# Performance work log

Hardware: AMD Instinct MI355X
Metric: run time of the kernel (lower is better)

## Reference

```python
import jax, jax.numpy as jnp
import numpy as np

B, N0, FEAT, NHID, GDIM = 32, 2048, 1036, 128, 32
DEG = 16
E = B * N0 * DEG
K1, K2, K3 = 410, 82, 17  # ceil(0.2*{2048,410,82}) per SAGPooling stage


def _segsum(v, idx, n):
    return jax.ops.segment_sum(v, idx, num_segments=n)


def sage_conv(x, src, dst, em, Wl, bl, Wr, n):
    # PyG SAGEConv: lin_l(mean_{j->i} x_j) + lin_r(x_i); lin applied before the
    # (linear) mean -> identical math, messages are NHID-dim not FEAT-dim.
    h = x @ Wl
    s = _segsum(h[src] * em[:, None], dst, n)
    cnt = _segsum(em, dst, n)
    return s / jnp.maximum(cnt, 1.0)[:, None] + bl + x @ Wr


def gcn_score(x, src, dst, em, W, b, n):
    # 1-channel GCNConv with self-loops and symmetric normalization.
    h = x @ W  # [n, 1]
    deg = 1.0 + _segsum(em, dst, n)  # +1 for self loop
    dis = jax.lax.rsqrt(deg)
    norm = dis[src] * dis[dst] * em
    agg = _segsum(h[src] * norm[:, None], dst, n) + h / deg[:, None]
    return (agg + b)[:, 0]


def sag_pool(x, src, dst, em, W, b, n_per, k):
    # Equal-size graphs -> static top-k per graph; dropped edges masked, not removed.
    nb = x.shape[0] // n_per
    score = gcn_score(x, src, dst, em, W, b, x.shape[0])
    _, idx = jax.lax.top_k(score.reshape(nb, n_per), k)
    perm = (idx + (jnp.arange(nb) * n_per)[:, None]).reshape(-1)
    xn = x[perm] * jnp.tanh(score[perm])[:, None]
    inv = jnp.full((x.shape[0],), -1, jnp.int32).at[perm].set(
        jnp.arange(nb * k, dtype=jnp.int32))
    ns, nd = inv[src], inv[dst]
    emn = em * ((ns >= 0) & (nd >= 0)).astype(em.dtype)
    return xn, jnp.maximum(ns, 0), jnp.maximum(nd, 0), emn


def readout(x, k):
    r = x.reshape(B, k, NHID)
    return jnp.concatenate([r.max(axis=1), r.mean(axis=1)], axis=1)  # [B, 2*NHID]


def graphnet(x, src, dst, W1l, b1l, W1r, Wp1, bp1, W2l, b2l, W2r, Wp2, bp2,
             W3l, b3l, W3r, Wp3, bp3, lin1_w, lin1_b, lin2_w, lin2_b, lin3_w, lin3_b):
    # NormalizeFeaturesV2: first 12 cols / column max
    mx = jnp.max(x[:, :12], axis=0)
    x = jnp.concatenate([x[:, :12] / mx, x[:, 12:]], axis=1)
    em = jnp.ones((E,), x.dtype)

    x = jax.nn.relu(sage_conv(x, src, dst, em, W1l, b1l, W1r, B * N0))
    x, s1, d1, e1 = sag_pool(x, src, dst, em, Wp1, bp1, N0, K1)
    x1 = readout(x, K1)

    x = jax.nn.relu(sage_conv(x, s1, d1, e1, W2l, b2l, W2r, B * K1))
    x, s2, d2, e2 = sag_pool(x, s1, d1, e1, Wp2, bp2, K1, K2)
    x2 = readout(x, K2)

    x = jax.nn.relu(sage_conv(x, s2, d2, e2, W3l, b3l, W3r, B * K2))
    x, s3, d3, e3 = sag_pool(x, s2, d2, e2, Wp3, bp3, K2, K3)
    x3 = readout(x, K3)

    h = x1 + x2 + x3
    h = jax.nn.relu(h @ lin1_w + lin1_b)  # dropout is identity at eval
    features = jax.nn.relu(h @ lin2_w + lin2_b)
    out = features @ lin3_w + lin3_b  # act=None
    return features, out


def setup_inputs():
    key = jax.random.key(0)
    ks = jax.random.split(key, 16)
    x = jax.random.normal(ks[0], (B * N0, FEAT), jnp.float32)
    e = jax.random.randint(ks[1], (2, B, N0 * DEG), 0, N0)
    ei = (e + (jnp.arange(B) * N0)[None, :, None]).reshape(2, -1).astype(jnp.int32)

    def lin(k, fi, fo):
        return (jax.random.normal(k, (fi, fo), jnp.float32) / np.sqrt(fi)).astype(jnp.float32)

    z = lambda *s: jnp.zeros(s, jnp.float32)
    return dict(
        x=x, src=ei[0], dst=ei[1],
        W1l=lin(ks[2], FEAT, NHID), b1l=z(NHID), W1r=lin(ks[3], FEAT, NHID),
        Wp1=lin(ks[4], NHID, 1), bp1=z(1),
        W2l=lin(ks[5], NHID, NHID), b2l=z(NHID), W2r=lin(ks[6], NHID, NHID),
        Wp2=lin(ks[7], NHID, 1), bp2=z(1),
        W3l=lin(ks[8], NHID, NHID), b3l=z(NHID), W3r=lin(ks[9], NHID, NHID),
        Wp3=lin(ks[10], NHID, 1), bp3=z(1),
        lin1_w=lin(ks[11], 2 * NHID, NHID), lin1_b=z(NHID),
        lin2_w=lin(ks[12], NHID, GDIM), lin2_b=z(GDIM),
        lin3_w=lin(ks[13], GDIM, 1), lin3_b=z(1),
    )


def reference(x, src, dst, W1l, b1l, W1r, Wp1, bp1, W2l, b2l, W2r, Wp2, bp2,
              W3l, b3l, W3r, Wp3, bp3, lin1_w, lin1_b, lin2_w, lin2_b, lin3_w, lin3_b):
    return graphnet(x, src, dst, W1l, b1l, W1r, Wp1, bp1, W2l, b2l, W2r, Wp2, bp2,
                    W3l, b3l, W3r, Wp3, bp3, lin1_w, lin1_b, lin2_w, lin2_b,
                    lin3_w, lin3_b)
```

## Files before the change

kernel.cpp:

```cpp
#include <hip/hip_runtime.h>

typedef unsigned int u32;
typedef unsigned short u16;

#define NB 32
#define N0V 2048
#define FEATV 1036
#define EDGESV (NB*N0V*16)
#define KK1 410
#define KK2 82
#define KK3 17
#define NN1 (NB*N0V)
#define NN2 (NB*KK1)
#define NN3 (NB*KK2)
#define NN4 (NB*KK3)
#define KSTEP1 33
#define KSTEP2 4
#define ESTR 32768

typedef __bf16 bf16x8 __attribute__((ext_vector_type(8)));
typedef float f32x4 __attribute__((ext_vector_type(4)));

__device__ inline u16 f2bf(float f){
  u32 u = __float_as_uint(f);
  u32 r = (u + 0x7FFFu + ((u >> 16) & 1u)) >> 16;
  return (u16)r;
}
__device__ inline float bf2f(u16 h){ return __uint_as_float(((u32)h) << 16); }
__device__ inline float dec_ord(u32 u){
  u32 bits = (u & 0x80000000u) ? (u ^ 0x80000000u) : ~u;
  return __uint_as_float(bits);
}
__device__ inline u16 bfbits(__bf16 b){ union{__bf16 f; u16 u;} c; c.f=b; return c.u; }
__device__ inline void cvt4c(float4 v, ushort4& h, ushort4& l){
  __bf16 h0=(__bf16)v.x, h1=(__bf16)v.y, h2=(__bf16)v.z, h3=(__bf16)v.w;
  float r0=v.x-(float)h0, r1=v.y-(float)h1, r2=v.z-(float)h2, r3=v.w-(float)h3;
  h.x=bfbits(h0); h.y=bfbits(h1); h.z=bfbits(h2); h.w=bfbits(h3);
  l.x=bfbits((__bf16)r0); l.y=bfbits((__bf16)r1);
  l.z=bfbits((__bf16)r2); l.w=bfbits((__bf16)r3);
}
__device__ inline void gload_lds16(const void* g, void* l){
  __builtin_amdgcn_global_load_lds(
      (const __attribute__((address_space(1))) unsigned int*)g,
      (__attribute__((address_space(3))) unsigned int*)l, 16, 0, 0);
}

__global__ void init_kernel(u32* mx){
  if (threadIdx.x < 12) mx[threadIdx.x] = 0;
}

__global__ void colmax_kernel(const float* __restrict__ x, u32* mx){
  __shared__ float sm[256];
  int t = threadIdx.x;
  int r = blockIdx.x*256 + t;
  const float4* p = (const float4*)(x + (size_t)r*FEATV);
  float4 v0 = p[0], v1 = p[1], v2 = p[2];
  float m[12] = {v0.x,v0.y,v0.z,v0.w, v1.x,v1.y,v1.z,v1.w, v2.x,v2.y,v2.z,v2.w};
  for (int j=0;j<12;j++){
    sm[t] = m[j]; __syncthreads();
    for (int off=128; off>0; off>>=1){ if (t<off) sm[t]=fmaxf(sm[t],sm[t+off]); __syncthreads(); }
    if (t==0){
      u32 b = __float_as_uint(sm[0]);
      u32 u = (b & 0x80000000u) ? ~b : (b | 0x80000000u);
      atomicMax(&mx[j], u);
    }
    __syncthreads();
  }
}

__global__ void wprep_all(const float* __restrict__ W1l, const float* __restrict__ W1r,
                          const float* __restrict__ W2l, const float* __restrict__ W2r,
                          const float* __restrict__ W3l, const float* __restrict__ W3r,
                          const u32* __restrict__ mxo,
                          u16* __restrict__ B1h, u16* __restrict__ B1l,
                          u16* __restrict__ B2h, u16* __restrict__ B2l,
                          u16* __restrict__ B3h, u16* __restrict__ B3l){
  int idx = blockIdx.x*256 + threadIdx.x;
  const float *Wl, *Wr; u16 *oh, *ol; int K, o, scale12;
  if (idx < KSTEP1*8192){ Wl=W1l; Wr=W1r; oh=B1h; ol=B1l; K=FEATV; o=idx; scale12=1; }
  else if (idx < (KSTEP1+KSTEP2)*8192){ Wl=W2l; Wr=W2r; oh=B2h; ol=B2l; K=128; o=idx-KSTEP1*8192; scale12=0; }
  else if (idx < (KSTEP1+2*KSTEP2)*8192){ Wl=W3l; Wr=W3r; oh=B3h; ol=B3l; K=128; o=idx-(KSTEP1+KSTEP2)*8192; scale12=0; }
  else return;
  int kt = o >> 13, r13 = o & 8191;
  int khg = r13 >> 11, n = (r13 >> 3) & 255, kk8 = r13 & 7;
  int k = (kt << 5) + khg*8 + kk8;
  float v = 0.f;
  if (k < K) v = (n < 128) ? Wl[(size_t)k*128 + n] : Wr[(size_t)k*128 + (n-128)];
  if (scale12 && k < 12) v /= dec_ord(mxo[k]);
  u16 h = f2bf(v);
  oh[o] = h;
  ol[o] = f2bf(v - bf2f(h));
}

__launch_bounds__(256, 2)
__global__ void gemm_csr_kernel(const float* __restrict__ A, int lda, int M,
                                int Kvalid, int Ksteps,
                                const u16* __restrict__ Bth, const u16* __restrict__ Btl,
                                float* __restrict__ hl, float* __restrict__ hr,
                                const int* __restrict__ sE, const int* __restrict__ dE,
                                const int* ecnt_in, int inGlobal, int nperIn, int nperOut,
                                const int* __restrict__ inv,
                                int* __restrict__ rps, int* __restrict__ rpd,
                                int* __restrict__ adjO, int* __restrict__ odstO,
                                int* __restrict__ ecnt_out){
  __shared__ __align__(16) u16 Ah[2][2048];
  __shared__ __align__(16) u16 Al[2][2048];
  __shared__ __align__(16) u16 Bh[2][8192];
  __shared__ __align__(16) u16 Bl[2][8192];
  int tid = threadIdx.x;

  if ((int)blockIdx.x < NB){
    int g = blockIdx.x;
    int* cnt  = (int*)&Bh[0][0];
    int* part = (int*)&Ah[0][0];
    int ne = ecnt_in ? ecnt_in[g] : ESTR;
    size_t eb = (size_t)g*ESTR;
    for (int i = tid; i < nperOut; i += 256) cnt[i] = 0;
    __syncthreads();
    for (int e = tid; e < ne; e += 256){
      int s = sE[eb+e], d = dE[eb+e];
      int ld; bool ok;
      if (inv){
        int gs = inGlobal ? s : g*nperIn + s;
        int gd = inGlobal ? d : g*nperIn + d;
        int ls = inv[gs]; ld = inv[gd];
        ok = (ls >= 0) && (ld >= 0);
      } else { ld = d - g*nperIn; ok = true; }
      if (ok) atomicAdd(&cnt[ld], 1);
    }
    __syncthreads();
    int chunk = (nperOut + 255) >> 8;
    int c0 = tid*chunk, ssum = 0;
    for (int u = 0; u < chunk; ++u){ int i = c0+u; if (i < nperOut) ssum += cnt[i]; }
    part[tid] = ssum;
    __syncthreads();
    for (int off = 1; off < 256; off <<= 1){
      int v = (tid >= off) ? part[tid-off] : 0;
      __syncthreads();
      part[tid] += v;
      __syncthreads();
    }
    int total = part[255];
    int run = part[tid] - ssum;
    for (int u = 0; u < chunk; ++u){
      int i = c0+u;
      if (i < nperOut){
        int c = cnt[i];
        rps[g*nperOut + i] = (int)(g*ESTR + run);
        rpd[g*nperOut + i] = c;
        cnt[i] = run;
        run += c;
      }
    }
    __syncthreads();
    for (int e = tid; e < ne; e += 256){
      int s = sE[eb+e], d = dE[eb+e];
      int ls, ld; bool ok;
      if (inv){
        int gs = inGlobal ? s : g*nperIn + s;
        int gd = inGlobal ? d : g*nperIn + d;
        ls = inv[gs]; ld = inv[gd];
        ok = (ls >= 0) && (ld >= 0);
      } else { ls = s - g*nperIn; ld = d - g*nperIn; ok = true; }
      if (ok){
        int p = atomicAdd(&cnt[ld], 1);
        adjO[eb + p] = ls;
        if (odstO) odstO[eb + p] = ld;
      }
    }
    if (ecnt_out && tid == 0) ecnt_out[g] = total;
    return;
  }

  int row0 = ((int)blockIdx.x - NB) * 64;
  int w = tid >> 6, lane = tid & 63;
  int lr = lane & 15, kh = lane >> 4;

  int p0i = tid, p1i = tid + 256;
  int kg0 = p0i >> 7, rw0 = (p0i & 127) >> 1, hf0 = p0i & 1;
  int kg1 = p1i >> 7, rw1 = (p1i & 127) >> 1, hf1 = p1i & 1;
  int coff0 = kg0*8 + hf0*4, coff1 = kg1*8 + hf1*4;
  const float* pA0 = A + (size_t)(row0 + rw0)*lda + coff0;
  const float* pA1 = A + (size_t)(row0 + rw1)*lda + coff1;
  int wi0 = kg0*512 + rw0*8 + hf0*4;
  int wi1 = kg1*512 + rw1*8 + hf1*4;

  f32x4 acc[4][4];
  #pragma unroll
  for (int i=0;i<4;i++)
    #pragma unroll
    for (int j=0;j<4;j++) acc[i][j] = (f32x4){0.f,0.f,0.f,0.f};

  float4 z4 = make_float4(0.f,0.f,0.f,0.f);

#define LOADA(KT, V0, V1) { int k0_ = (KT)<<5; \
    V0 = (k0_ + coff0 < Kvalid) ? *(const float4*)(pA0 + k0_) : z4; \
    V1 = (k0_ + coff1 < Kvalid) ? *(const float4*)(pA1 + k0_) : z4; }

#define ISSUEB(KT, BUF) { size_t tb_ = (size_t)(KT)*8192; \
    _Pragma("unroll") \
    for (int j_=0;j_<4;j_++){ int o_ = j_*2048 + w*512; \
      gload_lds16(Bth + tb_ + o_ + lane*8, &Bh[BUF][o_]); \
      gload_lds16(Btl + tb_ + o_ + lane*8, &Bl[BUF][o_]); } }

#define CVTWRITE(V0, V1, BUF) { ushort4 h_, l_; \
    cvt4c(V0, h_, l_); *(ushort4*)&Ah[BUF][wi0] = h_; *(ushort4*)&Al[BUF][wi0] = l_; \
    cvt4c(V1, h_, l_); *(ushort4*)&Ah[BUF][wi1] = h_; *(ushort4*)&Al[BUF][wi1] = l_; }

  float4 a0, a1, pp0, pp1;
  LOADA(0, a0, a1);
  ISSUEB(0, 0);
  LOADA(1, pp0, pp1);
  CVTWRITE(a0, a1, 0);
  asm volatile("s_waitcnt lgkmcnt(0)" ::: "memory");
  asm volatile("s_waitcnt vmcnt(2)" ::: "memory");
  __builtin_amdgcn_s_barrier();

  for (int kt = 0; kt < Ksteps; ++kt){
    int cur = kt & 1, nxt = cur ^ 1;
    if (kt+1 < Ksteps) ISSUEB(kt+1, nxt);
    float4 n0 = z4, n1 = z4;
    if (kt+2 < Ksteps) LOADA(kt+2, n0, n1);
    if (kt+2 < Ksteps)      asm volatile("s_waitcnt vmcnt(12)" ::: "memory");
    else if (kt+1 < Ksteps) asm volatile("s_waitcnt vmcnt(10)" ::: "memory");
    else                    asm volatile("s_waitcnt vmcnt(0)"  ::: "memory");

    bf16x8 fah[4], fal[4], fbh[4], fbl[4];
    #pragma unroll
    for (int mi=0;mi<4;mi++){
      int idx = kh*512 + (mi*16 + lr)*8;
      fah[mi] = *(const bf16x8*)&Ah[cur][idx];
      fal[mi] = *(const bf16x8*)&Al[cur][idx];
    }
    #pragma unroll
    for (int ni=0;ni<4;ni++){
      int idx = kh*2048 + (w*64 + ni*16 + lr)*8;
      fbh[ni] = *(const bf16x8*)&Bh[cur][idx];
      fbl[ni] = *(const bf16x8*)&Bl[cur][idx];
    }
    if (kt+1 < Ksteps) CVTWRITE(pp0, pp1, nxt);
    asm volatile("s_waitcnt lgkmcnt(0)" ::: "memory");
    __builtin_amdgcn_sched_barrier(0);
    __builtin_amdgcn_s_setprio(1);
    #pragma unroll
    for (int mi=0;mi<4;mi++)
      #pragma unroll
      for (int ni=0;ni<4;ni++){
        acc[mi][ni] = __builtin_amdgcn_mfma_f32_16x16x32_bf16(fah[mi], fbh[ni], acc[mi][ni], 0,0,0);
        acc[mi][ni] = __builtin_amdgcn_mfma_f32_16x16x32_bf16(fah[mi], fbl[ni], acc[mi][ni], 0,0,0);
        acc[mi][ni] = __builtin_amdgcn_mfma_f32_16x16x32_bf16(fal[mi], fbh[ni], acc[mi][ni], 0,0,0);
      }
    __builtin_amdgcn_s_setprio(0);
    pp0 = n0; pp1 = n1;
    __builtin_amdgcn_s_barrier();
  }
#undef LOADA
#undef ISSUEB
#undef CVTWRITE
  float* dst = (w < 2) ? hl : hr;
  #pragma unroll
  for (int mi=0;mi<4;mi++)
    #pragma unroll
    for (int j=0;j<4;j++){
      int row = row0 + mi*16 + kh*4 + j;
      #pragma unroll
      for (int ni=0;ni<4;ni++){
        int ch = (w*64 + ni*16 + lr) & 127;
        dst[(size_t)row*128 + ch] = acc[mi][ni][j];
      }
    }
}

__global__ void convfin_w(const float* __restrict__ hl, const float* __restrict__ hr,
                          const int* __restrict__ rps,
                          const int* __restrict__ rpd, const int* __restrict__ adj,
                          const float* __restrict__ bl, const float* __restrict__ Wp,
                          float* __restrict__ xout, float* __restrict__ hsc,
                          int nper, int bpg, int xcdMap){
  int b = blockIdx.x, t = threadIdx.x;
  int g, slot;
  if (xcdMap){ int xcd = b & 7, idx = b >> 3; g = xcd + 8*(idx >> 8); slot = idx & 255; }
  else { g = b / bpg; slot = b - g*bpg; }
  int wv = t >> 6, lane = t & 63;
  int sub = lane >> 5, l32 = lane & 31;
  int i = slot*8 + wv*2 + sub;
  if (i >= nper) return;
  int gbase = g*nper;
  int gi = gbase + i;
  int s = rps[gi], d = rpd[gi];
  const int* ap = adj + s;
  float4 a = make_float4(0.f,0.f,0.f,0.f);
  int e = 0;
  for (; e + 8 <= d; e += 8){
    int j0=ap[e],j1=ap[e+1],j2=ap[e+2],j3=ap[e+3];
    int j4=ap[e+4],j5=ap[e+5],j6=ap[e+6],j7=ap[e+7];
    float4 v0 = *(const float4*)(hl + (size_t)(gbase+j0)*128 + l32*4);
    float4 v1 = *(const float4*)(hl + (size_t)(gbase+j1)*128 + l32*4);
    float4 v2 = *(const float4*)(hl + (size_t)(gbase+j2)*128 + l32*4);
    float4 v3 = *(const float4*)(hl + (size_t)(gbase+j3)*128 + l32*4);
    float4 v4 = *(const float4*)(hl + (size_t)(gbase+j4)*128 + l32*4);
    float4 v5 = *(const float4*)(hl + (size_t)(gbase+j5)*128 + l32*4);
    float4 v6 = *(const float4*)(hl + (size_t)(gbase+j6)*128 + l32*4);
    float4 v7 = *(const float4*)(hl + (size_t)(gbase+j7)*128 + l32*4);
    a.x += v0.x+v1.x+v2.x+v3.x+v4.x+v5.x+v6.x+v7.x;
    a.y += v0.y+v1.y+v2.y+v3.y+v4.y+v5.y+v6.y+v7.y;
    a.z += v0.z+v1.z+v2.z+v3.z+v4.z+v5.z+v6.z+v7.z;
    a.w += v0.w+v1.w+v2.w+v3.w+v4.w+v5.w+v6.w+v7.w;
  }
  for (; e < d; ++e){
    float4 hj = *(const float4*)(hl + (size_t)(gbase + ap[e])*128 + l32*4);
    a.x += hj.x; a.y += hj.y; a.z += hj.z; a.w += hj.w;
  }
  float invc = 1.0f / fmaxf((float)d, 1.0f);
  float4 hrv = *(const float4*)(hr + (size_t)gi*128 + l32*4);
  float4 bb = *(const float4*)(bl + l32*4);
  float4 o;
  o.x = fmaxf(a.x*invc + bb.x + hrv.x, 0.f);
  o.y = fmaxf(a.y*invc + bb.y + hrv.y, 0.f);
  o.z = fmaxf(a.z*invc + bb.z + hrv.z, 0.f);
  o.w = fmaxf(a.w*invc + bb.w + hrv.w, 0.f);
  *(float4*)(xout + (size_t)gi*128 + l32*4) = o;
  float4 wp = *(const float4*)(Wp + l32*4);
  float v = o.x*wp.x + o.y*wp.y + o.z*wp.z + o.w*wp.w;
  #pragma unroll
  for (int m = 16; m > 0; m >>= 1) v += __shfl_xor(v, m);
  if (l32 == 0) hsc[gi] = v;
}

__global__ void scoreagg_w(const float* __restrict__ hsc, const int* __restrict__ rps,
                           const int* __restrict__ rpd, const int* __restrict__ adj,
                           const float* __restrict__ bp, int nper,
                           u32* __restrict__ su){
  int g = blockIdx.y;
  int i = blockIdx.x*256 + threadIdx.x;
  if (i >= nper) return;
  int gbase = g*nper;
  int gi = gbase + i;
  float di = 1.0f + (float)rpd[gi];
  float a = hsc[gi] / di;
  float rdi = rsqrtf(di);
  int s = rps[gi], d = rpd[gi];
  #pragma unroll 4
  for (int e = s; e < s+d; ++e){
    int j = gbase + adj[e];
    a += hsc[j] * rsqrtf(1.0f + (float)rpd[j]) * rdi;
  }
  float sc = a + bp[0];
  u32 b = __float_as_uint(sc);
  su[gi] = (b & 0x80000000u) ? ~b : (b | 0x80000000u);
}

__launch_bounds__(512)
__global__ void topkpool(const u32* __restrict__ suG, const float* __restrict__ xin,
                         int nper, int k,
                         float* __restrict__ xp, float* __restrict__ r,
                         int* __restrict__ invG){
  __shared__ u32 su[2048];
  __shared__ int bins[256], sfx[256];
  __shared__ int slist[416];
  __shared__ int tlist[64];
  __shared__ float smx[512], ssm[512];
  __shared__ u32 spfx;
  __shared__ int srem, ssel, stie;
  int g = blockIdx.x, t = threadIdx.x;
  int gbase = g*nper;
  for (int i = t; i < nper; i += 512){
    su[i] = suG[gbase + i];
    invG[gbase + i] = -1;
  }
  if (t == 0){ spfx = 0; srem = k; ssel = 0; stie = 0; }
  __syncthreads();
  for (int pass = 0; pass < 4; ++pass){
    int shift = 24 - 8*pass;
    if (t < 256) bins[t] = 0;
    __syncthreads();
    u32 pfx = spfx; int rem = srem;
    for (int i = t; i < nper; i += 512){
      u32 u = su[i];
      if (pass == 0 || (u >> (shift+8)) == (pfx >> (shift+8)))
        atomicAdd(&bins[(u >> shift) & 255], 1);
    }
    __syncthreads();
    if (t < 256) sfx[t] = bins[t];
    __syncthreads();
    for (int off=1; off<256; off<<=1){
      int v = 0;
      if (t < 256 && t + off < 256) v = sfx[t+off];
      __syncthreads();
      if (t < 256) sfx[t] += v;
      __syncthreads();
    }
    if (t < 256){
      int above = (t == 255) ? 0 : sfx[t+1];
      if (sfx[t] >= rem && above < rem){
        spfx = pfx | ((u32)t << shift);
        srem = rem - above;
      }
    }
    __syncthreads();
  }
  u32 th = spfx;
  for (int i = t; i < nper; i += 512)
    if (su[i] > th){ int p = atomicAdd(&ssel, 1); slist[p] = i; }
  __syncthreads();
  for (int i = t; i < nper; i += 512)
    if (su[i] == th){ int q = atomicAdd(&stie, 1); if (q < 64) tlist[q] = i; }
  __syncthreads();
  if (t == 0){
    int p = ssel, need = k - p;
    if (need > 0){
      if (stie <= 64){
        for (int a = 1; a < stie; ++a){
          int v = tlist[a], b2 = a-1;
          while (b2 >= 0 && tlist[b2] > v){ tlist[b2+1] = tlist[b2]; b2--; }
          tlist[b2+1] = v;
        }
        for (int m = 0; m < need; ++m) slist[p+m] = tlist[m];
      } else {
        for (int i = 0; i < nper && p < k; ++i)
          if (su[i] == th) slist[p++] = i;
      }
    }
  }
  __syncthreads();
  int q = t >> 7, c = t & 127;
  float mxv = -3.4e38f, smv = 0.f;
  for (int j = q; j < k; j += 4){
    int li = slist[j];
    float ts = tanhf(dec_ord(su[li]));
    float vv = xin[((size_t)(gbase + li))*128 + c] * ts;
    xp[((size_t)(g*k + j))*128 + c] = vv;
    mxv = fmaxf(mxv, vv); smv += vv;
  }
  smx[t] = mxv; ssm[t] = smv;
  for (int j = t; j < k; j += 512) invG[gbase + slist[j]] = j;
  __syncthreads();
  if (t < 128){
    r[g*256 + t] = fmaxf(fmaxf(smx[t], smx[t+128]), fmaxf(smx[t+256], smx[t+384]));
    r[g*256 + 128 + t] = (ssm[t]+ssm[t+128]+ssm[t+256]+ssm[t+384]) / (float)k;
  }
}

__global__ void head_kernel(const float* __restrict__ r1, const float* __restrict__ r2,
                            const float* __restrict__ r3,
                            const float* __restrict__ w1, const float* __restrict__ b1,
                            const float* __restrict__ w2, const float* __restrict__ b2,
                            const float* __restrict__ w3, const float* __restrict__ b3,
                            float* __restrict__ out){
  __shared__ float hs[32][256];
  __shared__ float h1[32][128];
  __shared__ float ft[32][32];
  int t = threadIdx.x;
  for (int o = t; o < 32*256; o += 256) hs[o>>8][o&255] = r1[o]+r2[o]+r3[o];
  __syncthreads();
  for (int o = t; o < 32*128; o += 256){
    int i = o >> 7, j = o & 127;
    float a = b1[j];
    for (int c = 0; c < 256; ++c) a += hs[i][c]*w1[c*128 + j];
    h1[i][j] = fmaxf(a, 0.f);
  }
  __syncthreads();
  for (int o = t; o < 32*32; o += 256){
    int i = o >> 5, j = o & 31;
    float a = b2[j];
    for (int c = 0; c < 128; ++c) a += h1[i][c]*w2[c*32 + j];
    float v = fmaxf(a, 0.f);
    ft[i][j] = v;
    out[o] = v;
  }
  __syncthreads();
  if (t < 32){
    float a = b3[0];
    for (int c = 0; c < 32; ++c) a += ft[t][c]*w3[c];
    out[1024 + t] = a;
  }
}

extern "C" void kernel_launch(void* const* d_in, const int* in_sizes, int n_in,
                              void* d_out, int out_size, void* d_ws, size_t ws_size,
                              hipStream_t stream){
  (void)in_sizes; (void)n_in; (void)out_size; (void)ws_size;
  const float* x   = (const float*)d_in[0];
  const int* esrc  = (const int*)d_in[1];
  const int* edst  = (const int*)d_in[2];
  const float* W1l = (const float*)d_in[3];
  const float* b1l = (const float*)d_in[4];
  const float* W1r = (const float*)d_in[5];
  const float* Wp1 = (const float*)d_in[6];
  const float* bp1 = (const float*)d_in[7];
  const float* W2l = (const float*)d_in[8];
  const float* b2l = (const float*)d_in[9];
  const float* W2r = (const float*)d_in[10];
  const float* Wp2 = (const float*)d_in[11];
  const float* bp2 = (const float*)d_in[12];
  const float* W3l = (const float*)d_in[13];
  const float* b3l = (const float*)d_in[14];
  const float* W3r = (const float*)d_in[15];
  const float* Wp3 = (const float*)d_in[16];
  const float* bp3 = (const float*)d_in[17];
  const float* l1w = (const float*)d_in[18];
  const float* l1b = (const float*)d_in[19];
  const float* l2w = (const float*)d_in[20];
  const float* l2b = (const float*)d_in[21];
  const float* l3w = (const float*)d_in[22];
  const float* l3b = (const float*)d_in[23];
  float* out = (float*)d_out;

  char* ws = (char*)d_ws;
  size_t off = 0;
  auto alloc = [&](size_t bytes)->char*{
    char* p = ws + off; off = (off + bytes + 255) & ~(size_t)255; return p;
  };

  u32* mx     = (u32*)alloc(64);
  int* ecntA  = (int*)alloc(NB*4);
  int* rps   = (int*)alloc((size_t)NN1*4);
  int* rpd   = (int*)alloc((size_t)NN1*4);
  int* adj1  = (int*)alloc((size_t)EDGESV*4);
  int* adjA  = (int*)alloc((size_t)EDGESV*4);
  int* odstA = (int*)alloc((size_t)EDGESV*4);
  int* adjB  = (int*)alloc((size_t)EDGESV*4);
  u16* B1h   = (u16*)alloc((size_t)KSTEP1*8192*2);
  u16* B1l   = (u16*)alloc((size_t)KSTEP1*8192*2);
  u16* B2h   = (u16*)alloc((size_t)KSTEP2*8192*2);
  u16* B2l   = (u16*)alloc((size_t)KSTEP2*8192*2);
  u16* B3h   = (u16*)alloc((size_t)KSTEP2*8192*2);
  u16* B3l   = (u16*)alloc((size_t)KSTEP2*8192*2);
  float* hlb = (float*)alloc((size_t)NN1*128*4);
  float* hrb = (float*)alloc((size_t)NN1*128*4);
  float* x1    = (float*)alloc((size_t)NN1*128*4);
  float* x2    = (float*)alloc((size_t)NN2*128*4);
  float* x3    = (float*)alloc((size_t)NN3*128*4);
  float* xp1   = (float*)alloc((size_t)NN2*128*4);
  float* xp2   = (float*)alloc((size_t)NN3*128*4);
  float* xp3   = (float*)alloc((size_t)NN4*128*4);
  float* hsc   = (float*)alloc((size_t)NN1*4);
  u32* suG     = (u32*)alloc((size_t)NN1*4);
  int* invG    = (int*)alloc((size_t)NN1*4);
  float* r1    = (float*)alloc((size_t)32*256*4);
  float* r2    = (float*)alloc((size_t)32*256*4);
  float* r3    = (float*)alloc((size_t)32*256*4);

  init_kernel<<<1, 64, 0, stream>>>(mx);
  colmax_kernel<<<256, 256, 0, stream>>>(x, mx);
  wprep_all<<<((KSTEP1+2*KSTEP2)*8192+255)/256, 256, 0, stream>>>(
      W1l, W1r, W2l, W2r, W3l, W3r, mx, B1h, B1l, B2h, B2l, B3h, B3l);

  gemm_csr_kernel<<<NB + NN1/64, 256, 0, stream>>>(
      x, FEATV, NN1, FEATV, KSTEP1, B1h, B1l, hlb, hrb,
      esrc, edst, nullptr, 1, N0V, N0V, nullptr,
      rps, rpd, adj1, nullptr, nullptr);
  convfin_w<<<NN1/8, 256, 0, stream>>>(hlb, hrb, rps, rpd, adj1, b1l, Wp1, x1, hsc, N0V, 256, 1);
  scoreagg_w<<<dim3(N0V/256, NB), 256, 0, stream>>>(hsc, rps, rpd, adj1, bp1, N0V, suG);
  topkpool<<<NB, 512, 0, stream>>>(suG, x1, N0V, KK1, xp1, r1, invG);

  gemm_csr_kernel<<<NB + NN2/64, 256, 0, stream>>>(
      xp1, 128, NN2, 128, KSTEP2, B2h, B2l, hlb, hrb,
      esrc, edst, nullptr, 1, N0V, KK1, invG,
      rps, rpd, adjA, odstA, ecntA);
  convfin_w<<<NB*52, 256, 0, stream>>>(hlb, hrb, rps, rpd, adjA, b2l, Wp2, x2, hsc, KK1, 52, 0);
  scoreagg_w<<<dim3((KK1+255)/256, NB), 256, 0, stream>>>(hsc, rps, rpd, adjA, bp2, KK1, suG);
  topkpool<<<NB, 512, 0, stream>>>(suG, x2, KK1, KK2, xp2, r2, invG);

  gemm_csr_kernel<<<NB + NN3/64, 256, 0, stream>>>(
      xp2, 128, NN3, 128, KSTEP2, B3h, B3l, hlb, hrb,
      adjA, odstA, ecntA, 0, KK1, KK2, invG,
      rps, rpd, adjB, nullptr, nullptr);
  convfin_w<<<NB*11, 256, 0, stream>>>(hlb, hrb, rps, rpd, adjB, b3l, Wp3, x3, hsc, KK2, 11, 0);
  scoreagg_w<<<dim3(1, NB), 256, 0, stream>>>(hsc, rps, rpd, adjB, bp3, KK2, suG);
  topkpool<<<NB, 512, 0, stream>>>(suG, x3, KK2, KK3, xp3, r3, invG);

  head_kernel<<<1, 256, 0, stream>>>(r1, r2, r3, l1w, l1b, l2w, l2b, l3w, l3b, out);
}
```

Baseline: 533.0 us.

## Stage neighbor features in LDS per graph for first-layer SAGE aggregation

Replaces the first-stage convfin_w with a kernel that loads an 8-channel slice of hl for a whole graph (2048 nodes) into shared memory. Each thread then aggregates neighbors for one node from LDS instead of gathering rows from global memory. Because the score projection was fused into the old kernel, it is split out into a separate warp-reduction GEMV kernel, which adds a launch and a re-read of x1. The shared array is 80 KB, which limits occupancy, and each block reads the adjacency lists 16 times (once per channel slice).

```diff
diff --git a/kernel.cpp b/kernel.cpp
--- a/kernel.cpp
+++ b/kernel.cpp
@@ -269,6 +269,71 @@
         dst[(size_t)row*128 + ch] = acc[mi][ni][j];
       }
     }
+}
+
+__launch_bounds__(256, 2)
+__global__ void convfin_lds(const float* __restrict__ hl, const float* __restrict__ hr,
+                            const int* __restrict__ rps, const int* __restrict__ rpd,
+                            const int* __restrict__ adj, const float* __restrict__ bl,
+                            float* __restrict__ xout){
+  __shared__ float sh[N0V*10];
+  int b = blockIdx.x;
+  int g = b >> 4, cc = b & 15;
+  int c0 = cc*8;
+  int t = threadIdx.x;
+  int gbase = g*N0V;
+  for (int r = t; r < N0V; r += 256){
+    const float* src = hl + (size_t)(gbase + r)*128 + c0;
+    float4 v0 = *(const float4*)(src);
+    float4 v1 = *(const float4*)(src+4);
+    float* d2 = &sh[r*10];
+    d2[0]=v0.x; d2[1]=v0.y; d2[2]=v0.z; d2[3]=v0.w;
+    d2[4]=v1.x; d2[5]=v1.y; d2[6]=v1.z; d2[7]=v1.w;
+  }
+  __syncthreads();
+  float bl0=bl[c0],bl1=bl[c0+1],bl2=bl[c0+2],bl3=bl[c0+3];
+  float bl4=bl[c0+4],bl5=bl[c0+5],bl6=bl[c0+6],bl7=bl[c0+7];
+  for (int i = t; i < N0V; i += 256){
+    int gi = gbase + i;
+    int s = rps[gi], d = rpd[gi];
+    float a0=0,a1=0,a2=0,a3=0,a4=0,a5=0,a6=0,a7=0;
+    const int* ap = adj + s;
+    for (int e = 0; e < d; ++e){
+      const float* row = &sh[ap[e]*10];
+      a0 += row[0]; a1 += row[1]; a2 += row[2]; a3 += row[3];
+      a4 += row[4]; a5 += row[5]; a6 += row[6]; a7 += row[7];
+    }
+    float invc = 1.0f / fmaxf((float)d, 1.0f);
+    const float* hrp = hr + (size_t)gi*128 + c0;
+    float4 h0 = *(const float4*)hrp;
+    float4 h1 = *(const float4*)(hrp+4);
+    float4 w0, w1;
+    w0.x = fmaxf(a0*invc + bl0 + h0.x, 0.f);
+    w0.y = fmaxf(a1*invc + bl1 + h0.y, 0.f);
+    w0.z = fmaxf(a2*invc + bl2 + h0.z, 0.f);
+    w0.w = fmaxf(a3*invc + bl3 + h0.w, 0.f);
+    w1.x = fmaxf(a4*invc + bl4 + h1.x, 0.f);
+    w1.y = fmaxf(a5*invc + bl5 + h1.y, 0.f);
+    w1.z = fmaxf(a6*invc + bl6 + h1.z, 0.f);
+    w1.w = fmaxf(a7*invc + bl7 + h1.w, 0.f);
+    float* xo = xout + (size_t)gi*128 + c0;
+    *(float4*)xo = w0;
+    *(float4*)(xo+4) = w1;
+  }
+}
+
+__global__ void hscgemv(const float* __restrict__ x1, const float* __restrict__ Wp,
+                        float* __restrict__ hsc){
+  int idx = blockIdx.x*256 + threadIdx.x;
+  int wv = idx >> 6, lane = idx & 63;
+  int sub = lane >> 5, l32 = lane & 31;
+  int node = wv*2 + sub;
+  float4 xv = *(const float4*)(x1 + (size_t)node*128 + l32*4);
+  float4 wp = *(const float4*)(Wp + l32*4);
+  float v = xv.x*wp.x + xv.y*wp.y + xv.z*wp.z + xv.w*wp.w;
+  #pragma unroll
+  for (int m = 16; m > 0; m >>= 1) v += __shfl_xor(v, m);
+  if (l32 == 0) hsc[node] = v;
 }
 
 __global__ void convfin_w(const float* __restrict__ hl, const float* __restrict__ hr,
@@ -550,7 +615,8 @@
       x, FEATV, NN1, FEATV, KSTEP1, B1h, B1l, hlb, hrb,
       esrc, edst, nullptr, 1, N0V, N0V, nullptr,
       rps, rpd, adj1, nullptr, nullptr);
-  convfin_w<<<NN1/8, 256, 0, stream>>>(hlb, hrb, rps, rpd, adj1, b1l, Wp1, x1, hsc, N0V, 256, 1);
+  convfin_lds<<<NB*16, 256, 0, stream>>>(hlb, hrb, rps, rpd, adj1, b1l, x1);
+  hscgemv<<<NN1/8, 256, 0, stream>>>(x1, Wp1, hsc);
   scoreagg_w<<<dim3(N0V/256, NB), 256, 0, stream>>>(hsc, rps, rpd, adj1, bp1, N0V, suG);
   topkpool<<<NB, 512, 0, stream>>>(suG, x1, N0V, KK1, xp1, r1, invG);
 
```

New measurement: 573.0 us. +7.5%, slower.

## Split CSR construction out of GEMM into grid-wide histogram, scan, scatter kernels

Applied to the files above, without the earlier changes.

Replaces the 32 per-graph CSR-building blocks that ran inside the GEMM launch with three separate kernels. These are a global-atomic degree histogram over all edges, a per-graph 1024-thread scan, and a global-atomic scatter. Each pooling stage now rebuilds its adjacency from the original edge list through chained inverse maps, instead of from the compacted previous stage. The intent is to remove the serial tail of 32 blocks each looping over 32K edges, which likely dominated the GEMM launch. The cost is extra launches, global atomics, and re-reading all edges at every stage.

```diff
diff --git a/kernel.cpp b/kernel.cpp
--- a/kernel.cpp
+++ b/kernel.cpp
@@ -47,6 +47,10 @@
 
 __global__ void init_kernel(u32* mx){
   if (threadIdx.x < 12) mx[threadIdx.x] = 0;
+}
+__global__ void fill0(int* p, int n){
+  int i = blockIdx.x*256 + threadIdx.x;
+  if (i < n) p[i] = 0;
 }
 
 __global__ void colmax_kernel(const float* __restrict__ x, u32* mx){
@@ -92,87 +96,83 @@
   ol[o] = f2bf(v - bf2f(h));
 }
 
+__global__ void histf(const int* __restrict__ src, const int* __restrict__ dst,
+                      const int* __restrict__ inv1, const int* __restrict__ inv2,
+                      int np1, int nperOut, int* __restrict__ deg){
+  int e = blockIdx.x*256 + threadIdx.x;
+  if (e >= EDGESV) return;
+  int s = src[e], d = dst[e];
+  int g = d >> 11;
+  int ls, ld;
+  if (inv1){
+    ls = inv1[s]; ld = inv1[d];
+    if ((ls | ld) < 0) return;
+    if (inv2){
+      ls = inv2[g*np1 + ls]; ld = inv2[g*np1 + ld];
+      if ((ls | ld) < 0) return;
+    }
+  } else { ld = d & 2047; }
+  atomicAdd(&deg[g*nperOut + ld], 1);
+}
+
+__launch_bounds__(1024)
+__global__ void scank(const int* __restrict__ deg, int nper,
+                      int* __restrict__ rps, int* __restrict__ cur){
+  __shared__ int part[1024];
+  int g = blockIdx.x, t = threadIdx.x;
+  int chunk = (nper + 1023) >> 10;
+  int c0 = t*chunk, ss = 0;
+  for (int u = 0; u < chunk; ++u){ int i = c0+u; if (i < nper) ss += deg[g*nper + i]; }
+  part[t] = ss; __syncthreads();
+  for (int off = 1; off < 1024; off <<= 1){
+    int v = (t >= off) ? part[t-off] : 0;
+    __syncthreads();
+    part[t] += v;
+    __syncthreads();
+  }
+  int run = part[t] - ss;
+  for (int u = 0; u < chunk; ++u){
+    int i = c0+u;
+    if (i < nper){
+      int pos = g*ESTR + run;
+      rps[g*nper + i] = pos;
+      cur[g*nper + i] = pos;
+      run += deg[g*nper + i];
+    }
+  }
+}
+
+__global__ void scatf(const int* __restrict__ src, const int* __restrict__ dst,
+                      const int* __restrict__ inv1, const int* __restrict__ inv2,
+                      int np1, int nperOut, int* __restrict__ cur, int* __restrict__ adj){
+  int e = blockIdx.x*256 + threadIdx.x;
+  if (e >= EDGESV) return;
+  int s = src[e], d = dst[e];
+  int g = d >> 11;
+  int ls, ld;
+  if (inv1){
+    ls = inv1[s]; ld = inv1[d];
+    if ((ls | ld) < 0) return;
+    if (inv2){
+      ls = inv2[g*np1 + ls]; ld = inv2[g*np1 + ld];
+      if ((ls | ld) < 0) return;
+    }
+  } else { ls = s & 2047; ld = d & 2047; }
+  int p = atomicAdd(&cur[g*nperOut + ld], 1);
+  adj[p] = ls;
+}
+
 __launch_bounds__(256, 2)
-__global__ void gemm_csr_kernel(const float* __restrict__ A, int lda, int M,
-                                int Kvalid, int Ksteps,
-                                const u16* __restrict__ Bth, const u16* __restrict__ Btl,
-                                float* __restrict__ hl, float* __restrict__ hr,
-                                const int* __restrict__ sE, const int* __restrict__ dE,
-                                const int* ecnt_in, int inGlobal, int nperIn, int nperOut,
-                                const int* __restrict__ inv,
-                                int* __restrict__ rps, int* __restrict__ rpd,
-                                int* __restrict__ adjO, int* __restrict__ odstO,
-                                int* __restrict__ ecnt_out){
+__global__ void gemm_kernel(const float* __restrict__ A, int lda,
+                            int Kvalid, int Ksteps,
+                            const u16* __restrict__ Bth, const u16* __restrict__ Btl,
+                            float* __restrict__ hl, float* __restrict__ hr){
   __shared__ __align__(16) u16 Ah[2][2048];
   __shared__ __align__(16) u16 Al[2][2048];
   __shared__ __align__(16) u16 Bh[2][8192];
   __shared__ __align__(16) u16 Bl[2][8192];
   int tid = threadIdx.x;
-
-  if ((int)blockIdx.x < NB){
-    int g = blockIdx.x;
-    int* cnt  = (int*)&Bh[0][0];
-    int* part = (int*)&Ah[0][0];
-    int ne = ecnt_in ? ecnt_in[g] : ESTR;
-    size_t eb = (size_t)g*ESTR;
-    for (int i = tid; i < nperOut; i += 256) cnt[i] = 0;
-    __syncthreads();
-    for (int e = tid; e < ne; e += 256){
-      int s = sE[eb+e], d = dE[eb+e];
-      int ld; bool ok;
-      if (inv){
-        int gs = inGlobal ? s : g*nperIn + s;
-        int gd = inGlobal ? d : g*nperIn + d;
-        int ls = inv[gs]; ld = inv[gd];
-        ok = (ls >= 0) && (ld >= 0);
-      } else { ld = d - g*nperIn; ok = true; }
-      if (ok) atomicAdd(&cnt[ld], 1);
-    }
-    __syncthreads();
-    int chunk = (nperOut + 255) >> 8;
-    int c0 = tid*chunk, ssum = 0;
-    for (int u = 0; u < chunk; ++u){ int i = c0+u; if (i < nperOut) ssum += cnt[i]; }
-    part[tid] = ssum;
-    __syncthreads();
-    for (int off = 1; off < 256; off <<= 1){
-      int v = (tid >= off) ? part[tid-off] : 0;
-      __syncthreads();
-      part[tid] += v;
-      __syncthreads();
-    }
-    int total = part[255];
-    int run = part[tid] - ssum;
-    for (int u = 0; u < chunk; ++u){
-      int i = c0+u;
-      if (i < nperOut){
-        int c = cnt[i];
-        rps[g*nperOut + i] = (int)(g*ESTR + run);
-        rpd[g*nperOut + i] = c;
-        cnt[i] = run;
-        run += c;
-      }
-    }
-    __syncthreads();
-    for (int e = tid; e < ne; e += 256){
-      int s = sE[eb+e], d = dE[eb+e];
-      int ls, ld; bool ok;
-      if (inv){
-        int gs = inGlobal ? s : g*nperIn + s;
-        int gd = inGlobal ? d : g*nperIn + d;
-        ls = inv[gs]; ld = inv[gd];
-        ok = (ls >= 0) && (ld >= 0);
-      } else { ls = s - g*nperIn; ld = d - g*nperIn; ok = true; }
-      if (ok){
-        int p = atomicAdd(&cnt[ld], 1);
-        adjO[eb + p] = ls;
-        if (odstO) odstO[eb + p] = ld;
-      }
-    }
-    if (ecnt_out && tid == 0) ecnt_out[g] = total;
-    return;
-  }
-
-  int row0 = ((int)blockIdx.x - NB) * 64;
+  int row0 = blockIdx.x * 64;
   int w = tid >> 6, lane = tid & 63;
   int lr = lane & 15, kh = lane >> 4;
 
@@ -512,14 +512,15 @@
     char* p = ws + off; off = (off + bytes + 255) & ~(size_t)255; return p;
   };
 
-  u32* mx     = (u32*)alloc(64);
-  int* ecntA  = (int*)alloc(NB*4);
+  u32* mx    = (u32*)alloc(64);
+  size_t z0 = off;
+  int* deg1  = (int*)alloc((size_t)NN1*4);
+  int* deg2  = (int*)alloc((size_t)NN2*4);
+  int* deg3  = (int*)alloc((size_t)NN3*4);
+  size_t zend = off;
   int* rps   = (int*)alloc((size_t)NN1*4);
-  int* rpd   = (int*)alloc((size_t)NN1*4);
-  int* adj1  = (int*)alloc((size_t)EDGESV*4);
-  int* adjA  = (int*)alloc((size_t)EDGESV*4);
-  int* odstA = (int*)alloc((size_t)EDGESV*4);
-  int* adjB  = (int*)alloc((size_t)EDGESV*4);
+  int* curB  = (int*)alloc((size_t)NN1*4);
+  int* adj   = (int*)alloc((size_t)EDGESV*4);
   u16* B1h   = (u16*)alloc((size_t)KSTEP1*8192*2);
   u16* B1l   = (u16*)alloc((size_t)KSTEP1*8192*2);
   u16* B2h   = (u16*)alloc((size_t)KSTEP2*8192*2);
@@ -536,39 +537,43 @@
   float* xp3   = (float*)alloc((size_t)NN4*128*4);
   float* hsc   = (float*)alloc((size_t)NN1*4);
   u32* suG     = (u32*)alloc((size_t)NN1*4);
-  int* invG    = (int*)alloc((size_t)NN1*4);
+  int* inv1G   = (int*)alloc((size_t)NN1*4);
+  int* inv2G   = (int*)alloc((size_t)NN2*4);
+  int* inv3G   = (int*)alloc((size_t)NN3*4);
   float* r1    = (float*)alloc((size_t)32*256*4);
   float* r2    = (float*)alloc((size_t)32*256*4);
   float* r3    = (float*)alloc((size_t)32*256*4);
 
+  int zn = (int)((zend - z0) / 4);
   init_kernel<<<1, 64, 0, stream>>>(mx);
+  fill0<<<(zn+255)/256, 256, 0, stream>>>((int*)(ws+z0), zn);
   colmax_kernel<<<256, 256, 0, stream>>>(x, mx);
   wprep_all<<<((KSTEP1+2*KSTEP2)*8192+255)/256, 256, 0, stream>>>(
       W1l, W1r, W2l, W2r, W3l, W3r, mx, B1h, B1l, B2h, B2l, B3h, B3l);
 
-  gemm_csr_kernel<<<NB + NN1/64, 256, 0, stream>>>(
-      x, FEATV, NN1, FEATV, KSTEP1, B1h, B1l, hlb, hrb,
-      esrc, edst, nullptr, 1, N0V, N0V, nullptr,
-      rps, rpd, adj1, nullptr, nullptr);
-  convfin_w<<<NN1/8, 256, 0, stream>>>(hlb, hrb, rps, rpd, adj1, b1l, Wp1, x1, hsc, N0V, 256, 1);
-  scoreagg_w<<<dim3(N0V/256, NB), 256, 0, stream>>>(hsc, rps, rpd, adj1, bp1, N0V, suG);
-  topkpool<<<NB, 512, 0, stream>>>(suG, x1, N0V, KK1, xp1, r1, invG);
-
-  gemm_csr_kernel<<<NB + NN2/64, 256, 0, stream>>>(
-      xp1, 128, NN2, 128, KSTEP2, B2h, B2l, hlb, hrb,
-      esrc, edst, nullptr, 1, N0V, KK1, invG,
-      rps, rpd, adjA, odstA, ecntA);
-  convfin_w<<<NB*52, 256, 0, stream>>>(hlb, hrb, rps, rpd, adjA, b2l, Wp2, x2, hsc, KK1, 52, 0);
-  scoreagg_w<<<dim3((KK1+255)/256, NB), 256, 0, stream>>>(hsc, rps, rpd, adjA, bp2, KK1, suG);
-  topkpool<<<NB, 512, 0, stream>>>(suG, x2, KK1, KK2, xp2, r2, invG);
-
-  gemm_csr_kernel<<<NB + NN3/64, 256, 0, stream>>>(
-      xp2, 128, NN3, 128, KSTEP2, B3h, B3l, hlb, hrb,
-      adjA, odstA, ecntA, 0, KK1, KK2, invG,
-      rps, rpd, adjB, nullptr, nullptr);
-  convfin_w<<<NB*11, 256, 0, stream>>>(hlb, hrb, rps, rpd, adjB, b3l, Wp3, x3, hsc, KK2, 11, 0);
-  scoreagg_w<<<dim3(1, NB), 256, 0, stream>>>(hsc, rps, rpd, adjB, bp3, KK2, suG);
-  topkpool<<<NB, 512, 0, stream>>>(suG, x3, KK2, KK3, xp3, r3, invG);
+  histf<<<EDGESV/256, 256, 0, stream>>>(esrc, edst, nullptr, nullptr, 0, N0V, deg1);
+  scank<<<NB, 1024, 0, stream>>>(deg1, N0V, rps, curB);
+  scatf<<<EDGESV/256, 256, 0, stream>>>(esrc, edst, nullptr, nullptr, 0, N0V, curB, adj);
+  gemm_kernel<<<NN1/64, 256, 0, stream>>>(x, FEATV, FEATV, KSTEP1, B1h, B1l, hlb, hrb);
+  convfin_w<<<NN1/8, 256, 0, stream>>>(hlb, hrb, rps, deg1, adj, b1l, Wp1, x1, hsc, N0V, 256, 1);
+  scoreagg_w<<<dim3(N0V/256, NB), 256, 0, stream>>>(hsc, rps, deg1, adj, bp1, N0V, suG);
+  topkpool<<<NB, 512, 0, stream>>>(suG, x1, N0V, KK1, xp1, r1, inv1G);
+
+  histf<<<EDGESV/256, 256, 0, stream>>>(esrc, edst, inv1G, nullptr, 0, KK1, deg2);
+  scank<<<NB, 1024, 0, stream>>>(deg2, KK1, rps, curB);
+  scatf<<<EDGESV/256, 256, 0, stream>>>(esrc, edst, inv1G, nullptr, 0, KK1, curB, adj);
+  gemm_kernel<<<NN2/64, 256, 0, stream>>>(xp1, 128, 128, KSTEP2, B2h, B2l, hlb, hrb);
+  convfin_w<<<NB*52, 256, 0, stream>>>(hlb, hrb, rps, deg2, adj, b2l, Wp2, x2, hsc, KK1, 52, 0);
+  scoreagg_w<<<dim3((KK1+255)/256, NB), 256, 0, stream>>>(hsc, rps, deg2, adj, bp2, KK1, suG);
+  topkpool<<<NB, 512, 0, stream>>>(suG, x2, KK1, KK2, xp2, r2, inv2G);
+
+  histf<<<EDGESV/256, 256, 0, stream>>>(esrc, edst, inv1G, inv2G, KK1, KK2, deg3);
+  scank<<<NB, 1024, 0, stream>>>(deg3, KK2, rps, curB);
+  scatf<<<EDGESV/256, 256, 0, stream>>>(esrc, edst, inv1G, inv2G, KK1, KK2, curB, adj);
+  gemm_kernel<<<NN3/64, 256, 0, stream>>>(xp2, 128, 128, KSTEP2, B3h, B3l, hlb, hrb);
+  convfin_w<<<NB*11, 256, 0, stream>>>(hlb, hrb, rps, deg3, adj, b3l, Wp3, x3, hsc, KK2, 11, 0);
+  scoreagg_w<<<dim3(1, NB), 256, 0, stream>>>(hsc, rps, deg3, adj, bp3, KK2, suG);
+  topkpool<<<NB, 512, 0, stream>>>(suG, x3, KK2, KK3, xp3, r3, inv3G);
 
   head_kernel<<<1, 256, 0, stream>>>(r1, r2, r3, l1w, l1b, l2w, l2b, l3w, l3b, out);
 }
```

Result: no change. 527.0 us (-1.1%).
